# Optimization experiments

Measured on AMD Instinct MI355X. Metric: run time of the kernel, lower is better.

## Reference

```python
import jax, jax.numpy as jnp
import numpy as np

N = 50000   # nodes
E = 800000  # edges (avg degree 16)
D = 128     # feature / hidden dim


def _lin(x, W, b):
    # torch nn.Linear convention: W is [out, in]
    return x @ W.T + b


def setup_inputs() -> dict:
    key = jax.random.key(0)
    ks = jax.random.split(key, 24)
    p = lambda k, s: jax.random.normal(k, s, dtype=jnp.float32) * 0.05
    inp = {
        "node_feat": jax.random.normal(ks[0], (N, D), dtype=jnp.float32),
        "edge_feat": jax.random.normal(ks[1], (E, D), dtype=jnp.float32),
        "src_idx": jax.random.randint(ks[2], (E,), 0, N),
        "dst_idx": jax.random.randint(ks[3], (E,), 0, N),
        "Wsrc": p(ks[4], (D, D)), "bsrc": p(ks[5], (D,)),
        "Wdst": p(ks[6], (D, D)), "bdst": p(ks[7], (D,)),
        "Wphi1": p(ks[8], (D, D)), "bphi1": p(ks[9], (D,)),
        "Wphi2": p(ks[10], (D, D)), "bphi2": p(ks[11], (D,)),
        "Wphi3": p(ks[12], (D, D)), "bphi3": p(ks[13], (D,)),
        "Wth1": p(ks[14], (D, D)), "bth1": p(ks[15], (D,)),
        "Wth2": p(ks[16], (D, D)), "bth2": p(ks[17], (D,)),
        "Wpd": p(ks[18], (D, D)), "bpd": p(ks[19], (D,)),
        "Wpu": p(ks[20], (D, D)), "bpu": p(ks[21], (D,)),
    }
    return inp


def reference(node_feat, edge_feat, src_idx, dst_idx,
              Wsrc, bsrc, Wdst, bdst,
              Wphi1, bphi1, Wphi2, bphi2, Wphi3, bphi3,
              Wth1, bth1, Wth2, bth2,
              Wpd, bpd, Wpu, bpu):
    h = node_feat                               # [N, D]
    h_src = h[src_idx]                          # [E, D] gather
    h_dst = h[dst_idx]                          # [E, D] gather
    # edge code: e + affine(src) + affine(dst)
    t = edge_feat + _lin(h_src, Wsrc, bsrc) + _lin(h_dst, Wdst, bdst)
    # phi MLP (activation_first=True, n_hidden=2): ReLU, L, ReLU, L, ReLU, L
    x = jax.nn.relu(t)
    x = jax.nn.relu(_lin(x, Wphi1, bphi1))
    x = jax.nn.relu(_lin(x, Wphi2, bphi2))
    e_emb = _lin(x, Wphi3, bphi3)               # [E, D]
    # u_mul_e + sum: message = h[src] * e_emb, scatter-sum into dst
    m = h_src * e_emb                           # [E, D]
    agg = jax.ops.segment_sum(m, dst_idx, num_segments=h.shape[0])  # [N, D]
    # combine: theta(phi_dst(h) + phi_upd(agg)); theta = ReLU, L, ReLU, L
    y = _lin(h, Wpd, bpd) + _lin(agg, Wpu, bpu)
    y = jax.nn.relu(y)
    y = jax.nn.relu(_lin(y, Wth1, bth1))
    return _lin(y, Wth2, bth2)                  # [N, D]
```

## Files before the change

### kernel.cpp

```cpp
#include <hip/hip_runtime.h>
#include <hip/hip_bf16.h>

#define NN 50000
#define NE 800000
#define NT_E 12500

typedef __attribute__((ext_vector_type(8))) short bf16x8;
typedef __attribute__((ext_vector_type(4))) float f32x4;
typedef __attribute__((ext_vector_type(8))) unsigned short u16x8;

__device__ __forceinline__ unsigned short f2bf(float f) {
    union { float f; unsigned u; } v; v.f = f;
    unsigned r = v.u + 0x7FFFu + ((v.u >> 16) & 1u);
    return (unsigned short)(r >> 16);
}
__device__ __forceinline__ float bf2f(unsigned short h) {
    union { unsigned u; float f; } v; v.u = ((unsigned)h) << 16;
    return v.f;
}
__device__ __forceinline__ f32x4 mfma16(bf16x8 a, bf16x8 b, f32x4 c) {
    return __builtin_amdgcn_mfma_f32_16x16x32_bf16(a, b, c, 0, 0, 0);
}

__device__ __forceinline__ void load_wfrags(const unsigned short* __restrict__ Wb,
                                            int wv, int lane, bf16x8 (&wf)[4][2]) {
#pragma unroll
    for (int kk = 0; kk < 4; ++kk)
#pragma unroll
        for (int j = 0; j < 2; ++j) {
            int row = 32 * wv + 16 * j + (lane & 15);
            int col = 32 * kk + 8 * (lane >> 4);
            wf[kk][j] = *(const bf16x8*)(Wb + row * 128 + col);
        }
}

__device__ __forceinline__ void zero_acc(f32x4 (&acc)[4][2]) {
#pragma unroll
    for (int mt = 0; mt < 4; ++mt)
#pragma unroll
        for (int j = 0; j < 2; ++j) {
            f32x4 z = {0.f, 0.f, 0.f, 0.f};
            acc[mt][j] = z;
        }
}

__device__ __forceinline__ void gemm64(const unsigned short* __restrict__ X,
                                       const bf16x8 (&wf)[4][2], f32x4 (&acc)[4][2], int lane) {
#pragma unroll
    for (int kk = 0; kk < 4; ++kk) {
        bf16x8 a[4];
#pragma unroll
        for (int mt = 0; mt < 4; ++mt) {
            int row = mt * 16 + (lane & 15);
            a[mt] = *(const bf16x8*)(X + row * 136 + kk * 32 + 8 * (lane >> 4));
        }
#pragma unroll
        for (int mt = 0; mt < 4; ++mt) {
            acc[mt][0] = mfma16(a[mt], wf[kk][0], acc[mt][0]);
            acc[mt][1] = mfma16(a[mt], wf[kk][1], acc[mt][1]);
        }
    }
}

__device__ __forceinline__ void epi_lds(unsigned short* __restrict__ Xo,
                                        const f32x4 (&acc)[4][2],
                                        float bb0, float bb1, int c0, int rbase) {
#pragma unroll
    for (int mt = 0; mt < 4; ++mt)
#pragma unroll
        for (int r = 0; r < 4; ++r) {
            int row = mt * 16 + rbase + r;
            Xo[row * 136 + c0]      = f2bf(fmaxf(acc[mt][0][r] + bb0, 0.f));
            Xo[row * 136 + c0 + 16] = f2bf(fmaxf(acc[mt][1][r] + bb1, 0.f));
        }
}

__global__ void k_wconv(const float* w0, const float* w1, const float* w2,
                        const float* w3, const float* w4, const float* w5,
                        const float* w6, const float* w7, const float* w8,
                        unsigned short* out) {
    const float* ws[9] = {w0, w1, w2, w3, w4, w5, w6, w7, w8};
    int m = blockIdx.x >> 2;
    int part = blockIdx.x & 3;
    const float* w = ws[m] + part * 4096 + threadIdx.x * 16;
    unsigned short* o = out + m * 16384 + part * 4096 + threadIdx.x * 16;
    float f[16];
#pragma unroll
    for (int i = 0; i < 4; ++i) *(f32x4*)(f + 4 * i) = ((const f32x4*)w)[i];
    unsigned short tmp[16];
#pragma unroll
    for (int i = 0; i < 16; ++i) tmp[i] = f2bf(f[i]);
    ((u16x8*)o)[0] = *(u16x8*)tmp;
    ((u16x8*)o)[1] = *(u16x8*)(tmp + 8);
}

__global__ __launch_bounds__(256, 2)
void k_nodepre(const float* __restrict__ h,
               const unsigned short* __restrict__ Wb,
               const float* __restrict__ bsrc, const float* __restrict__ bdst,
               unsigned short* __restrict__ Asrc, unsigned short* __restrict__ Adst,
               unsigned short* __restrict__ Hb) {
    __shared__ unsigned short X[64 * 136];
    int tid = threadIdx.x, lane = tid & 63, wv = tid >> 6;
    int n0 = blockIdx.x * 64;
    {
        int row = tid >> 2, q = tid & 3;
        int n = n0 + row;
        unsigned short tmp[32];
        if (n < NN) {
            const f32x4* hp = (const f32x4*)(h + (size_t)n * 128 + q * 32);
#pragma unroll
            for (int i = 0; i < 8; ++i) {
                f32x4 v = hp[i];
#pragma unroll
                for (int j = 0; j < 4; ++j) tmp[i * 4 + j] = f2bf(v[j]);
            }
        } else {
#pragma unroll
            for (int i = 0; i < 32; ++i) tmp[i] = 0;
        }
#pragma unroll
        for (int i = 0; i < 4; ++i)
            *(u16x8*)(X + row * 136 + q * 32 + i * 8) = *(u16x8*)(tmp + i * 8);
        if (n < NN) {
            u16x8* hb = (u16x8*)(Hb + (size_t)n * 128 + q * 32);
#pragma unroll
            for (int i = 0; i < 4; ++i) hb[i] = *(u16x8*)(tmp + i * 8);
        }
    }
    __syncthreads();

    bf16x8 wfS[4][2], wfD[4][2];
    load_wfrags(Wb, wv, lane, wfS);
    load_wfrags(Wb + 16384, wv, lane, wfD);
    f32x4 accS[4][2], accD[4][2];
    zero_acc(accS); zero_acc(accD);
    gemm64(X, wfS, accS, lane);
    gemm64(X, wfD, accD, lane);

    int c0 = 32 * wv + (lane & 15);
    float bs0 = bsrc[c0], bs1 = bsrc[c0 + 16];
    float bd0 = bdst[c0], bd1 = bdst[c0 + 16];
    int rbase = (lane >> 4) * 4;
#pragma unroll
    for (int mt = 0; mt < 4; ++mt)
#pragma unroll
        for (int r = 0; r < 4; ++r) {
            int n = n0 + mt * 16 + rbase + r;
            if (n < NN) {
                size_t o = (size_t)n * 128;
                Asrc[o + c0]      = f2bf(accS[mt][0][r] + bs0);
                Asrc[o + c0 + 16] = f2bf(accS[mt][1][r] + bs1);
                Adst[o + c0]      = f2bf(accD[mt][0][r] + bd0);
                Adst[o + c0 + 16] = f2bf(accD[mt][1][r] + bd1);
            }
        }
}

__global__ __launch_bounds__(256, 2)
void k_edge(const float* __restrict__ ef,
            const int* __restrict__ src, const int* __restrict__ dst,
            const unsigned short* __restrict__ Asrc,
            const unsigned short* __restrict__ Adst,
            const unsigned short* __restrict__ Hb,
            const unsigned short* __restrict__ Wb,
            const float* __restrict__ b1, const float* __restrict__ b2,
            const float* __restrict__ b3,
            float* __restrict__ agg) {
    __shared__ unsigned short X0[64 * 136];
    __shared__ unsigned short X1[64 * 136];
    __shared__ unsigned short Hs[64 * 136];
    __shared__ int soff_lds[64];
    __shared__ int doff_lds[64];

    int tid = threadIdx.x, lane = tid & 63, wv = tid >> 6;

    bf16x8 wf1[4][2], wf2[4][2], wf3[4][2];
    load_wfrags(Wb + 2 * 16384, wv, lane, wf1);
    load_wfrags(Wb + 3 * 16384, wv, lane, wf2);
    load_wfrags(Wb + 4 * 16384, wv, lane, wf3);

    int c0 = 32 * wv + (lane & 15);
    float b1_0 = b1[c0], b1_1 = b1[c0 + 16];
    float b2_0 = b2[c0], b2_1 = b2[c0 + 16];
    float b3_0 = b3[c0], b3_1 = b3[c0 + 16];
    int rbase = (lane >> 4) * 4;
    int srow = tid >> 2, q = tid & 3;

    for (int t = blockIdx.x; t < NT_E; t += gridDim.x) {
        int e0 = t * 64;
        __syncthreads();
        if (tid < 64) {
            soff_lds[tid] = src[e0 + tid] * 128;
            doff_lds[tid] = dst[e0 + tid] * 128;
        }
        __syncthreads();
        {
            int so = soff_lds[srow], dofs = doff_lds[srow];
            const f32x4* ep = (const f32x4*)(ef + (size_t)(e0 + srow) * 128 + q * 32);
            const u16x8* ap = (const u16x8*)(Asrc + so + q * 32);
            const u16x8* dp = (const u16x8*)(Adst + dofs + q * 32);
            const u16x8* hp = (const u16x8*)(Hb + so + q * 32);
#pragma unroll
            for (int i = 0; i < 4; ++i) {
                u16x8 a8 = ap[i], d8 = dp[i], h8 = hp[i];
                f32x4 e_lo = ep[2 * i], e_hi = ep[2 * i + 1];
                unsigned short o[8];
#pragma unroll
                for (int j = 0; j < 8; ++j) {
                    float evv = (j < 4) ? e_lo[j] : e_hi[j - 4];
                    float v = evv + bf2f((unsigned short)a8[j]) + bf2f((unsigned short)d8[j]);
                    o[j] = f2bf(fmaxf(v, 0.f));
                }
                *(u16x8*)(X0 + srow * 136 + q * 32 + i * 8) = *(u16x8*)o;
                *(u16x8*)(Hs + srow * 136 + q * 32 + i * 8) = h8;
            }
        }
        __syncthreads();
        f32x4 acc[4][2];
        zero_acc(acc);
        gemm64(X0, wf1, acc, lane);
        __syncthreads();
        epi_lds(X1, acc, b1_0, b1_1, c0, rbase);
        __syncthreads();
        zero_acc(acc);
        gemm64(X1, wf2, acc, lane);
        epi_lds(X0, acc, b2_0, b2_1, c0, rbase);
        __syncthreads();
        zero_acc(acc);
        gemm64(X0, wf3, acc, lane);
#pragma unroll
        for (int mt = 0; mt < 4; ++mt)
#pragma unroll
            for (int r = 0; r < 4; ++r) {
                int row = mt * 16 + rbase + r;
                int dofs = doff_lds[row];
                float h0 = bf2f(Hs[row * 136 + c0]);
                float h1 = bf2f(Hs[row * 136 + c0 + 16]);
                atomicAdd(agg + dofs + c0,      (acc[mt][0][r] + b3_0) * h0);
                atomicAdd(agg + dofs + c0 + 16, (acc[mt][1][r] + b3_1) * h1);
            }
    }
}

__global__ __launch_bounds__(256, 2)
void k_nodeout(const unsigned short* __restrict__ Hb,
               const float* __restrict__ agg,
               const unsigned short* __restrict__ Wb,
               const float* __restrict__ bpd, const float* __restrict__ bpu,
               const float* __restrict__ bt1, const float* __restrict__ bt2,
               float* __restrict__ out) {
    __shared__ unsigned short Xh[64 * 136];
    __shared__ unsigned short Xa[64 * 136];
    int tid = threadIdx.x, lane = tid & 63, wv = tid >> 6;
    int n0 = blockIdx.x * 64;
    {
        int row = tid >> 2, q = tid & 3;
        int n = n0 + row;
        if (n < NN) {
            const u16x8* hp = (const u16x8*)(Hb + (size_t)n * 128 + q * 32);
#pragma unroll
            for (int i = 0; i < 4; ++i)
                *(u16x8*)(Xh + row * 136 + q * 32 + i * 8) = hp[i];
            const f32x4* gp = (const f32x4*)(agg + (size_t)n * 128 + q * 32);
#pragma unroll
            for (int i = 0; i < 4; ++i) {
                f32x4 lo = gp[2 * i], hi = gp[2 * i + 1];
                unsigned short tmp[8];
#pragma unroll
                for (int j = 0; j < 4; ++j) { tmp[j] = f2bf(lo[j]); tmp[4 + j] = f2bf(hi[j]); }
                *(u16x8*)(Xa + row * 136 + q * 32 + i * 8) = *(u16x8*)tmp;
            }
        } else {
            u16x8 z = {0, 0, 0, 0, 0, 0, 0, 0};
#pragma unroll
            for (int i = 0; i < 4; ++i) {
                *(u16x8*)(Xh + row * 136 + q * 32 + i * 8) = z;
                *(u16x8*)(Xa + row * 136 + q * 32 + i * 8) = z;
            }
        }
    }
    __syncthreads();
    bf16x8 wfa[4][2], wfb[4][2];
    load_wfrags(Wb + 5 * 16384, wv, lane, wfa);
    load_wfrags(Wb + 6 * 16384, wv, lane, wfb);
    int c0 = 32 * wv + (lane & 15);
    int rbase = (lane >> 4) * 4;
    f32x4 acc[4][2];
    zero_acc(acc);
    gemm64(Xh, wfa, acc, lane);
    gemm64(Xa, wfb, acc, lane);
    float bb0 = bpd[c0] + bpu[c0], bb1 = bpd[c0 + 16] + bpu[c0 + 16];
    __syncthreads();
    epi_lds(Xh, acc, bb0, bb1, c0, rbase);
    __syncthreads();
    load_wfrags(Wb + 7 * 16384, wv, lane, wfa);
    zero_acc(acc);
    gemm64(Xh, wfa, acc, lane);
    float b10 = bt1[c0], b11 = bt1[c0 + 16];
    __syncthreads();
    epi_lds(Xa, acc, b10, b11, c0, rbase);
    __syncthreads();
    load_wfrags(Wb + 8 * 16384, wv, lane, wfb);
    zero_acc(acc);
    gemm64(Xa, wfb, acc, lane);
    float b20 = bt2[c0], b21 = bt2[c0 + 16];
#pragma unroll
    for (int mt = 0; mt < 4; ++mt)
#pragma unroll
        for (int r = 0; r < 4; ++r) {
            int n = n0 + mt * 16 + rbase + r;
            if (n < NN) {
                out[(size_t)n * 128 + c0]      = acc[mt][0][r] + b20;
                out[(size_t)n * 128 + c0 + 16] = acc[mt][1][r] + b21;
            }
        }
}

extern "C" void kernel_launch(void* const* d_in, const int* in_sizes, int n_in,
                              void* d_out, int out_size, void* d_ws, size_t ws_size,
                              hipStream_t stream) {
    (void)in_sizes; (void)n_in; (void)out_size; (void)ws_size;
    const float* node_feat = (const float*)d_in[0];
    const float* edge_feat = (const float*)d_in[1];
    const int*   src  = (const int*)d_in[2];
    const int*   dst  = (const int*)d_in[3];
    const float* Wsrc = (const float*)d_in[4];  const float* bsrc = (const float*)d_in[5];
    const float* Wdst = (const float*)d_in[6];  const float* bdst = (const float*)d_in[7];
    const float* Wphi1 = (const float*)d_in[8]; const float* bphi1 = (const float*)d_in[9];
    const float* Wphi2 = (const float*)d_in[10];const float* bphi2 = (const float*)d_in[11];
    const float* Wphi3 = (const float*)d_in[12];const float* bphi3 = (const float*)d_in[13];
    const float* Wth1 = (const float*)d_in[14]; const float* bth1 = (const float*)d_in[15];
    const float* Wth2 = (const float*)d_in[16]; const float* bth2 = (const float*)d_in[17];
    const float* Wpd  = (const float*)d_in[18]; const float* bpd  = (const float*)d_in[19];
    const float* Wpu  = (const float*)d_in[20]; const float* bpu  = (const float*)d_in[21];

    char* ws = (char*)d_ws;
    unsigned short* Wb   = (unsigned short*)ws;
    unsigned short* Asrc = (unsigned short*)(ws + 294912);
    unsigned short* Adst = (unsigned short*)(ws + 294912 + 12800000);
    unsigned short* Hb   = (unsigned short*)(ws + 294912 + 25600000);
    float*          agg  = (float*)(ws + 294912 + 38400000);

    hipMemsetAsync(agg, 0, (size_t)NN * 128 * 4, stream);

    k_wconv<<<36, 256, 0, stream>>>(Wsrc, Wdst, Wphi1, Wphi2, Wphi3,
                                    Wpd, Wpu, Wth1, Wth2, Wb);
    k_nodepre<<<782, 256, 0, stream>>>(node_feat, Wb, bsrc, bdst, Asrc, Adst, Hb);
    k_edge<<<1024, 256, 0, stream>>>(edge_feat, src, dst, Asrc, Adst, Hb, Wb,
                                     bphi1, bphi2, bphi3, agg);
    k_nodeout<<<782, 256, 0, stream>>>(Hb, agg, Wb, bpd, bpu, bth1, bth2, (float*)d_out);
}
```

Baseline: 468.3 us.

## Sort edges by destination and pre-reduce messages in LDS before atomics

Builds a destination-sorted edge permutation each call using a histogram, a single-block scan and an atomic-cursor scatter. The edge kernel then processes edges in that order with contiguous tile ranges per block, and reduces runs of equal destinations through shared memory so far fewer global atomics hit agg. It also drops the bf16 copy of node features: the edge kernel gathers fp32 node_feat directly and converts it, and occupancy rises to 3 blocks. Costs are three extra small kernels, indirect, uncoalesced reads of edge_feat through the permutation, and wider fp32 gathers for h_src.

```diff
diff --git a/kernel.cpp b/kernel.cpp
--- a/kernel.cpp
+++ b/kernel.cpp
@@ -73,6 +73,18 @@
             Xo[row * 136 + c0]      = f2bf(fmaxf(acc[mt][0][r] + bb0, 0.f));
             Xo[row * 136 + c0 + 16] = f2bf(fmaxf(acc[mt][1][r] + bb1, 0.f));
         }
+}
+
+__device__ __forceinline__ void stage_f32row(unsigned short* __restrict__ Xrow,
+                                             const f32x4* __restrict__ p) {
+#pragma unroll
+    for (int i = 0; i < 4; ++i) {
+        f32x4 lo = p[2 * i], hi = p[2 * i + 1];
+        unsigned short tmp[8];
+#pragma unroll
+        for (int j = 0; j < 4; ++j) { tmp[j] = f2bf(lo[j]); tmp[4 + j] = f2bf(hi[j]); }
+        *(u16x8*)(Xrow + i * 8) = *(u16x8*)tmp;
+    }
 }
 
 __global__ void k_wconv(const float* w0, const float* w1, const float* w2,
@@ -94,38 +106,62 @@
     ((u16x8*)o)[1] = *(u16x8*)(tmp + 8);
 }
 
-__global__ __launch_bounds__(256, 2)
+__global__ void k_hist(const int* __restrict__ dst, int* __restrict__ cnt) {
+    int i = blockIdx.x * 256 + threadIdx.x;
+    int stride = gridDim.x * 256;
+    for (; i < NE; i += stride) atomicAdd(&cnt[dst[i]], 1);
+}
+
+__global__ void k_scan(int* __restrict__ c) {
+    __shared__ int part[1024];
+    int tid = threadIdx.x;
+    const int CH = 49;
+    int base = tid * CH;
+    int s = 0;
+    for (int i = 0; i < CH; ++i) { int idx = base + i; if (idx < NN) s += c[idx]; }
+    part[tid] = s;
+    __syncthreads();
+    for (int off = 1; off < 1024; off <<= 1) {
+        int v = (tid >= off) ? part[tid - off] : 0;
+        __syncthreads();
+        part[tid] += v;
+        __syncthreads();
+    }
+    int excl = (tid == 0) ? 0 : part[tid - 1];
+    for (int i = 0; i < CH; ++i) {
+        int idx = base + i;
+        if (idx < NN) { int cc = c[idx]; c[idx] = excl; excl += cc; }
+    }
+}
+
+__global__ void k_perm(const int* __restrict__ dst, int* __restrict__ cursor,
+                       int* __restrict__ perm) {
+    int i = blockIdx.x * 256 + threadIdx.x;
+    int stride = gridDim.x * 256;
+    for (; i < NE; i += stride) {
+        int p = atomicAdd(&cursor[dst[i]], 1);
+        perm[p] = i;
+    }
+}
+
+__global__ __launch_bounds__(256, 3)
 void k_nodepre(const float* __restrict__ h,
                const unsigned short* __restrict__ Wb,
                const float* __restrict__ bsrc, const float* __restrict__ bdst,
-               unsigned short* __restrict__ Asrc, unsigned short* __restrict__ Adst,
-               unsigned short* __restrict__ Hb) {
+               unsigned short* __restrict__ Asrc, unsigned short* __restrict__ Adst) {
     __shared__ unsigned short X[64 * 136];
     int tid = threadIdx.x, lane = tid & 63, wv = tid >> 6;
     int n0 = blockIdx.x * 64;
     {
         int row = tid >> 2, q = tid & 3;
         int n = n0 + row;
-        unsigned short tmp[32];
         if (n < NN) {
-            const f32x4* hp = (const f32x4*)(h + (size_t)n * 128 + q * 32);
-#pragma unroll
-            for (int i = 0; i < 8; ++i) {
-                f32x4 v = hp[i];
-#pragma unroll
-                for (int j = 0; j < 4; ++j) tmp[i * 4 + j] = f2bf(v[j]);
-            }
+            stage_f32row(X + row * 136 + q * 32,
+                         (const f32x4*)(h + (size_t)n * 128 + q * 32));
         } else {
-#pragma unroll
-            for (int i = 0; i < 32; ++i) tmp[i] = 0;
-        }
-#pragma unroll
-        for (int i = 0; i < 4; ++i)
-            *(u16x8*)(X + row * 136 + q * 32 + i * 8) = *(u16x8*)(tmp + i * 8);
-        if (n < NN) {
-            u16x8* hb = (u16x8*)(Hb + (size_t)n * 128 + q * 32);
-#pragma unroll
-            for (int i = 0; i < 4; ++i) hb[i] = *(u16x8*)(tmp + i * 8);
+            u16x8 z = {0, 0, 0, 0, 0, 0, 0, 0};
+#pragma unroll
+            for (int i = 0; i < 4; ++i) *(u16x8*)(X + row * 136 + q * 32 + i * 8) = z;
         }
     }
     __syncthreads();
@@ -157,21 +193,25 @@
         }
 }
 
-__global__ __launch_bounds__(256, 2)
+__global__ __launch_bounds__(256, 3)
 void k_edge(const float* __restrict__ ef,
+            const float* __restrict__ nf,
             const int* __restrict__ src, const int* __restrict__ dst,
+            const int* __restrict__ perm,
             const unsigned short* __restrict__ Asrc,
             const unsigned short* __restrict__ Adst,
-            const unsigned short* __restrict__ Hb,
             const unsigned short* __restrict__ Wb,
             const float* __restrict__ b1, const float* __restrict__ b2,
             const float* __restrict__ b3,
             float* __restrict__ agg) {
-    __shared__ unsigned short X0[64 * 136];
-    __shared__ unsigned short X1[64 * 136];
-    __shared__ unsigned short Hs[64 * 136];
-    __shared__ int soff_lds[64];
-    __shared__ int doff_lds[64];
+    __shared__ __align__(16) char sh[52992];
+    unsigned short* X0 = (unsigned short*)sh;
+    unsigned short* X1 = (unsigned short*)(sh + 17408);
+    float*          Mf = (float*)sh;
+    unsigned short* Hs = (unsigned short*)(sh + 34816);
+    int* soff = (int*)(sh + 52224);
+    int* didx = (int*)(sh + 52480);
+    int* eidx = (int*)(sh + 52736);
 
     int tid = threadIdx.x, lane = tid & 63, wv = tid >> 6;
 
@@ -187,33 +227,45 @@
     int rbase = (lane >> 4) * 4;
     int srow = tid >> 2, q = tid & 3;
 
-    for (int t = blockIdx.x; t < NT_E; t += gridDim.x) {
+    int b = blockIdx.x, nb = gridDim.x;
+    int qt = NT_E / nb, rt = NT_E % nb;
+    int t0 = (b < rt) ? b * (qt + 1) : rt * (qt + 1) + (b - rt) * qt;
+    int t1 = t0 + ((b < rt) ? qt + 1 : qt);
+
+    for (int t = t0; t < t1; ++t) {
         int e0 = t * 64;
         __syncthreads();
         if (tid < 64) {
-            soff_lds[tid] = src[e0 + tid] * 128;
-            doff_lds[tid] = dst[e0 + tid] * 128;
+            int e = perm[e0 + tid];
+            eidx[tid] = e;
+            soff[tid] = src[e] * 128;
+            didx[tid] = dst[e];
         }
         __syncthreads();
         {
-            int so = soff_lds[srow], dofs = doff_lds[srow];
-            const f32x4* ep = (const f32x4*)(ef + (size_t)(e0 + srow) * 128 + q * 32);
+            int e = eidx[srow];
+            int so = soff[srow];
+            int dofs = didx[srow] * 128;
+            const f32x4* ep = (const f32x4*)(ef + (size_t)e * 128 + q * 32);
+            const f32x4* hp = (const f32x4*)(nf + (size_t)so + q * 32);
             const u16x8* ap = (const u16x8*)(Asrc + so + q * 32);
             const u16x8* dp = (const u16x8*)(Adst + dofs + q * 32);
-            const u16x8* hp = (const u16x8*)(Hb + so + q * 32);
 #pragma unroll
             for (int i = 0; i < 4; ++i) {
-                u16x8 a8 = ap[i], d8 = dp[i], h8 = hp[i];
+                u16x8 a8 = ap[i], d8 = dp[i];
                 f32x4 e_lo = ep[2 * i], e_hi = ep[2 * i + 1];
-                unsigned short o[8];
+                f32x4 h_lo = hp[2 * i], h_hi = hp[2 * i + 1];
+                unsigned short o[8], hb[8];
 #pragma unroll
                 for (int j = 0; j < 8; ++j) {
                     float evv = (j < 4) ? e_lo[j] : e_hi[j - 4];
+                    float hv  = (j < 4) ? h_lo[j] : h_hi[j - 4];
                     float v = evv + bf2f((unsigned short)a8[j]) + bf2f((unsigned short)d8[j]);
                     o[j] = f2bf(fmaxf(v, 0.f));
+                    hb[j] = f2bf(hv);
                 }
                 *(u16x8*)(X0 + srow * 136 + q * 32 + i * 8) = *(u16x8*)o;
-                *(u16x8*)(Hs + srow * 136 + q * 32 + i * 8) = h8;
+                *(u16x8*)(Hs + srow * 136 + q * 32 + i * 8) = *(u16x8*)hb;
             }
         }
         __syncthreads();
@@ -229,22 +281,38 @@
         __syncthreads();
         zero_acc(acc);
         gemm64(X0, wf3, acc, lane);
+        __syncthreads();
 #pragma unroll
         for (int mt = 0; mt < 4; ++mt)
 #pragma unroll
             for (int r = 0; r < 4; ++r) {
                 int row = mt * 16 + rbase + r;
-                int dofs = doff_lds[row];
                 float h0 = bf2f(Hs[row * 136 + c0]);
                 float h1 = bf2f(Hs[row * 136 + c0 + 16]);
-                atomicAdd(agg + dofs + c0,      (acc[mt][0][r] + b3_0) * h0);
-                atomicAdd(agg + dofs + c0 + 16, (acc[mt][1][r] + b3_1) * h1);
-            }
-    }
-}
-
-__global__ __launch_bounds__(256, 2)
-void k_nodeout(const unsigned short* __restrict__ Hb,
+                Mf[row * 128 + c0]      = (acc[mt][0][r] + b3_0) * h0;
+                Mf[row * 128 + c0 + 16] = (acc[mt][1][r] + b3_1) * h1;
+            }
+        __syncthreads();
+        {
+            int col = tid & 127;
+            int r0 = (tid >> 7) * 32;
+            float s = 0.f;
+            int cur = didx[r0];
+            for (int r = r0; r < r0 + 32; ++r) {
+                int d2 = didx[r];
+                if (d2 != cur) {
+                    atomicAdd(agg + (size_t)cur * 128 + col, s);
+                    s = 0.f; cur = d2;
+                }
+                s += Mf[r * 128 + col];
+            }
+            atomicAdd(agg + (size_t)cur * 128 + col, s);
+        }
+    }
+}
+
+__global__ __launch_bounds__(256, 3)
+void k_nodeout(const float* __restrict__ h,
                const float* __restrict__ agg,
                const unsigned short* __restrict__ Wb,
                const float* __restrict__ bpd, const float* __restrict__ bpu,
@@ -258,19 +326,10 @@
         int row = tid >> 2, q = tid & 3;
         int n = n0 + row;
         if (n < NN) {
-            const u16x8* hp = (const u16x8*)(Hb + (size_t)n * 128 + q * 32);
-#pragma unroll
-            for (int i = 0; i < 4; ++i)
-                *(u16x8*)(Xh + row * 136 + q * 32 + i * 8) = hp[i];
-            const f32x4* gp = (const f32x4*)(agg + (size_t)n * 128 + q * 32);
-#pragma unroll
-            for (int i = 0; i < 4; ++i) {
-                f32x4 lo = gp[2 * i], hi = gp[2 * i + 1];
-                unsigned short tmp[8];
-#pragma unroll
-                for (int j = 0; j < 4; ++j) { tmp[j] = f2bf(lo[j]); tmp[4 + j] = f2bf(hi[j]); }
-                *(u16x8*)(Xa + row * 136 + q * 32 + i * 8) = *(u16x8*)tmp;
-            }
+            stage_f32row(Xh + row * 136 + q * 32,
+                         (const f32x4*)(h + (size_t)n * 128 + q * 32));
+            stage_f32row(Xa + row * 136 + q * 32,
+                         (const f32x4*)(agg + (size_t)n * 128 + q * 32));
         } else {
             u16x8 z = {0, 0, 0, 0, 0, 0, 0, 0};
 #pragma unroll
@@ -338,16 +397,22 @@
     char* ws = (char*)d_ws;
     unsigned short* Wb   = (unsigned short*)ws;
     unsigned short* Asrc = (unsigned short*)(ws + 294912);
-    unsigned short* Adst = (unsigned short*)(ws + 294912 + 12800000);
-    unsigned short* Hb   = (unsigned short*)(ws + 294912 + 25600000);
-    float*          agg  = (float*)(ws + 294912 + 38400000);
+    unsigned short* Adst = (unsigned short*)(ws + 13094912);
+    float*          agg  = (float*)(ws + 25894912);
+    int*            perm = (int*)(ws + 51494912);
+    int*            cnt  = (int*)(ws + 54694912);
 
     hipMemsetAsync(agg, 0, (size_t)NN * 128 * 4, stream);
+    hipMemsetAsync(cnt, 0, (size_t)NN * 4, stream);
 
     k_wconv<<<36, 256, 0, stream>>>(Wsrc, Wdst, Wphi1, Wphi2, Wphi3,
                                     Wpd, Wpu, Wth1, Wth2, Wb);
-    k_nodepre<<<782, 256, 0, stream>>>(node_feat, Wb, bsrc, bdst, Asrc, Adst, Hb);
-    k_edge<<<1024, 256, 0, stream>>>(edge_feat, src, dst, Asrc, Adst, Hb, Wb,
-                                     bphi1, bphi2, bphi3, agg);
-    k_nodeout<<<782, 256, 0, stream>>>(Hb, agg, Wb, bpd, bpu, bth1, bth2, (float*)d_out);
-}
+    k_hist<<<1024, 256, 0, stream>>>(dst, cnt);
+    k_scan<<<1, 1024, 0, stream>>>(cnt);
+    k_perm<<<1024, 256, 0, stream>>>(dst, cnt, perm);
+    k_nodepre<<<782, 256, 0, stream>>>(node_feat, Wb, bsrc, bdst, Asrc, Adst);
+    k_edge<<<1024, 256, 0, stream>>>(edge_feat, node_feat, src, dst, perm,
+                                     Asrc, Adst, Wb, bphi1, bphi2, bphi3, agg);
+    k_nodeout<<<782, 256, 0, stream>>>(node_feat, agg, Wb, bpd, bpu, bth1, bth2,
+                                       (float*)d_out);
+}
```

Result: slower. 923.9 us (+97.3%).

## Replace atomic scatter with CSR-sorted message buffer and segmented reduction

Applied to the files above, without the earlier changes.

Builds a CSR of destinations each call (histogram, three-stage scan, position assignment). The edge kernel writes bf16 messages into a dst-sorted buffer instead of issuing float atomics, and a separate per-node kernel then sums each segment without atomics. The edge kernel also prefetches the next tile's gathers into registers to overlap them with the MLP, and occupancy hints rise to 3 blocks. This costs extra launches, a large extra buffer of writes and reads, and bf16 rounding of messages. It falls back to the atomic path when the workspace is too small.

```diff
diff --git a/kernel.cpp b/kernel.cpp
--- a/kernel.cpp
+++ b/kernel.cpp
@@ -4,10 +4,14 @@
 #define NN 50000
 #define NE 800000
 #define NT_E 12500
+#define GRID_E 1536
+#define NBLK_SCAN 196
 
 typedef __attribute__((ext_vector_type(8))) short bf16x8;
 typedef __attribute__((ext_vector_type(4))) float f32x4;
+typedef __attribute__((ext_vector_type(2))) float f32x2;
 typedef __attribute__((ext_vector_type(8))) unsigned short u16x8;
+typedef __attribute__((ext_vector_type(2))) unsigned short u16x2;
 
 __device__ __forceinline__ unsigned short f2bf(float f) {
     union { float f; unsigned u; } v; v.f = f;
@@ -21,6 +25,9 @@
 __device__ __forceinline__ f32x4 mfma16(bf16x8 a, bf16x8 b, f32x4 c) {
     return __builtin_amdgcn_mfma_f32_16x16x32_bf16(a, b, c, 0, 0, 0);
 }
+__device__ __forceinline__ void syncl() {
+    asm volatile("s_waitcnt lgkmcnt(0)\n\ts_barrier" ::: "memory");
+}
 
 __device__ __forceinline__ void load_wfrags(const unsigned short* __restrict__ Wb,
                                             int wv, int lane, bf16x8 (&wf)[4][2]) {
@@ -73,6 +80,18 @@
             Xo[row * 136 + c0]      = f2bf(fmaxf(acc[mt][0][r] + bb0, 0.f));
             Xo[row * 136 + c0 + 16] = f2bf(fmaxf(acc[mt][1][r] + bb1, 0.f));
         }
+}
+
+__device__ __forceinline__ void stage_f32row(unsigned short* __restrict__ Xrow,
+                                             const f32x4* __restrict__ p) {
+#pragma unroll
+    for (int i = 0; i < 4; ++i) {
+        f32x4 lo = p[2 * i], hi = p[2 * i + 1];
+        unsigned short tmp[8];
+#pragma unroll
+        for (int j = 0; j < 4; ++j) { tmp[j] = f2bf(lo[j]); tmp[4 + j] = f2bf(hi[j]); }
+        *(u16x8*)(Xrow + i * 8) = *(u16x8*)tmp;
+    }
 }
 
 __global__ void k_wconv(const float* w0, const float* w1, const float* w2,
@@ -94,7 +113,63 @@
     ((u16x8*)o)[1] = *(u16x8*)(tmp + 8);
 }
 
-__global__ __launch_bounds__(256, 2)
+__global__ void k_hist(const int* __restrict__ dst, int* __restrict__ cnt) {
+    int i = blockIdx.x * 256 + threadIdx.x;
+    if (i < NE) atomicAdd(&cnt[dst[i]], 1);
+}
+
+__global__ void k_scan1(const int* __restrict__ c, int* __restrict__ bsum) {
+    __shared__ int red[256];
+    int i = blockIdx.x * 256 + threadIdx.x;
+    red[threadIdx.x] = (i < NN) ? c[i] : 0;
+    __syncthreads();
+    for (int off = 128; off > 0; off >>= 1) {
+        if (threadIdx.x < off) red[threadIdx.x] += red[threadIdx.x + off];
+        __syncthreads();
+    }
+    if (threadIdx.x == 0) bsum[blockIdx.x] = red[0];
+}
+
+__global__ void k_scan2(int* __restrict__ bsum) {
+    __shared__ int s[256];
+    int t = threadIdx.x;
+    s[t] = (t < NBLK_SCAN) ? bsum[t] : 0;
+    __syncthreads();
+    for (int off = 1; off < 256; off <<= 1) {
+        int v = (t >= off) ? s[t - off] : 0;
+        __syncthreads();
+        s[t] += v;
+        __syncthreads();
+    }
+    if (t < NBLK_SCAN) bsum[t] = (t == 0) ? 0 : s[t - 1];
+}
+
+__global__ void k_scan3(int* __restrict__ cnt, const int* __restrict__ bsum,
+                        int* __restrict__ rowptr) {
+    __shared__ int s[256];
+    int t = threadIdx.x;
+    int i = blockIdx.x * 256 + t;
+    int v = (i < NN) ? cnt[i] : 0;
+    s[t] = v;
+    __syncthreads();
+    for (int off = 1; off < 256; off <<= 1) {
+        int x = (t >= off) ? s[t - off] : 0;
+        __syncthreads();
+        s[t] += x;
+        __syncthreads();
+    }
+    int excl = bsum[blockIdx.x] + s[t] - v;
+    if (i < NN) { rowptr[i] = excl; cnt[i] = excl; }
+    if (i == 0) rowptr[NN] = NE;
+}
+
+__global__ void k_pos(const int* __restrict__ dst, int* __restrict__ cursor,
+                      int* __restrict__ pos) {
+    int i = blockIdx.x * 256 + threadIdx.x;
+    if (i < NE) pos[i] = atomicAdd(&cursor[dst[i]], 1);
+}
+
+__global__ __launch_bounds__(256, 3)
 void k_nodepre(const float* __restrict__ h,
                const unsigned short* __restrict__ Wb,
                const float* __restrict__ bsrc, const float* __restrict__ bdst,
@@ -106,8 +181,8 @@
     {
         int row = tid >> 2, q = tid & 3;
         int n = n0 + row;
-        unsigned short tmp[32];
         if (n < NN) {
+            unsigned short tmp[32];
             const f32x4* hp = (const f32x4*)(h + (size_t)n * 128 + q * 32);
 #pragma unroll
             for (int i = 0; i < 8; ++i) {
@@ -115,17 +190,16 @@
 #pragma unroll
                 for (int j = 0; j < 4; ++j) tmp[i * 4 + j] = f2bf(v[j]);
             }
+#pragma unroll
+            for (int i = 0; i < 4; ++i)
+                *(u16x8*)(X + row * 136 + q * 32 + i * 8) = *(u16x8*)(tmp + i * 8);
+            u16x8* hb = (u16x8*)(Hb + (size_t)n * 128 + q * 32);
+#pragma unroll
+            for (int i = 0; i < 4; ++i) hb[i] = *(u16x8*)(tmp + i * 8);
         } else {
-#pragma unroll
-            for (int i = 0; i < 32; ++i) tmp[i] = 0;
-        }
-#pragma unroll
-        for (int i = 0; i < 4; ++i)
-            *(u16x8*)(X + row * 136 + q * 32 + i * 8) = *(u16x8*)(tmp + i * 8);
-        if (n < NN) {
-            u16x8* hb = (u16x8*)(Hb + (size_t)n * 128 + q * 32);
-#pragma unroll
-            for (int i = 0; i < 4; ++i) hb[i] = *(u16x8*)(tmp + i * 8);
+            u16x8 z = {0, 0, 0, 0, 0, 0, 0, 0};
+#pragma unroll
+            for (int i = 0; i < 4; ++i) *(u16x8*)(X + row * 136 + q * 32 + i * 8) = z;
         }
     }
     __syncthreads();
@@ -157,16 +231,156 @@
         }
 }
 
+__global__ __launch_bounds__(256, 3)
+void k_edgeA(const float* __restrict__ ef,
+             const int* __restrict__ src, const int* __restrict__ dst,
+             const int* __restrict__ pos,
+             const unsigned short* __restrict__ Asrc,
+             const unsigned short* __restrict__ Adst,
+             const unsigned short* __restrict__ Hb,
+             const unsigned short* __restrict__ Wb,
+             const float* __restrict__ b1, const float* __restrict__ b2,
+             const float* __restrict__ b3,
+             unsigned short* __restrict__ Mbuf) {
+    __shared__ __align__(16) char sh[52480];
+    unsigned short* X0 = (unsigned short*)sh;
+    unsigned short* X1 = (unsigned short*)(sh + 17408);
+    unsigned short* Hs = (unsigned short*)(sh + 34816);
+    float*          Mf = (float*)sh;
+    int*         posarr = (int*)(sh + 52224);
+
+    int tid = threadIdx.x, lane = tid & 63, wv = tid >> 6;
+
+    bf16x8 wf1[4][2], wf2[4][2], wf3[4][2];
+    load_wfrags(Wb + 2 * 16384, wv, lane, wf1);
+    load_wfrags(Wb + 3 * 16384, wv, lane, wf2);
+    load_wfrags(Wb + 4 * 16384, wv, lane, wf3);
+
+    int c0 = 32 * wv + (lane & 15);
+    float b1_0 = b1[c0], b1_1 = b1[c0 + 16];
+    float b2_0 = b2[c0], b2_1 = b2[c0 + 16];
+    float b3_0 = b3[c0], b3_1 = b3[c0 + 16];
+    int rbase = (lane >> 4) * 4;
+    int srow = tid >> 2, q = tid & 3;
+
+    int e_nx, s_nx, d_nx, p_nx;
+    f32x4 efr[8];
+    u16x8 asr[4], adr[4], hbr[4];
+
+    auto load_idx = [&](int t) {
+        int e = t * 64 + srow;
+        e_nx = e;
+        s_nx = src[e]; d_nx = dst[e]; p_nx = pos[e];
+    };
+    auto load_gather = [&]() {
+        const f32x4* ep = (const f32x4*)(ef + (size_t)e_nx * 128 + q * 32);
+#pragma unroll
+        for (int i = 0; i < 8; ++i) efr[i] = ep[i];
+        const u16x8* ap = (const u16x8*)(Asrc + (size_t)s_nx * 128 + q * 32);
+        const u16x8* dp = (const u16x8*)(Adst + (size_t)d_nx * 128 + q * 32);
+        const u16x8* hp = (const u16x8*)(Hb + (size_t)s_nx * 128 + q * 32);
+#pragma unroll
+        for (int i = 0; i < 4; ++i) { asr[i] = ap[i]; adr[i] = dp[i]; hbr[i] = hp[i]; }
+    };
+
+    int t0 = blockIdx.x;
+    load_idx(t0);
+    load_gather();
+
+    for (int t = t0; t < NT_E; t += GRID_E) {
+        int tn = t + GRID_E;
+        syncl();
+        {
+#pragma unroll
+            for (int i = 0; i < 4; ++i) {
+                u16x8 a8 = asr[i], d8 = adr[i];
+                f32x4 lo = efr[2 * i], hi = efr[2 * i + 1];
+                unsigned short o[8];
+#pragma unroll
+                for (int j = 0; j < 8; ++j) {
+                    float evv = (j < 4) ? lo[j] : hi[j - 4];
+                    float v = evv + bf2f((unsigned short)a8[j]) + bf2f((unsigned short)d8[j]);
+                    o[j] = f2bf(fmaxf(v, 0.f));
+                }
+                *(u16x8*)(X0 + srow * 136 + q * 32 + i * 8) = *(u16x8*)o;
+                *(u16x8*)(Hs + srow * 136 + q * 32 + i * 8) = hbr[i];
+            }
+            if (q == 0) posarr[srow] = p_nx;
+        }
+        if (tn < NT_E) load_idx(tn);
+        syncl();
+        if (tn < NT_E) load_gather();
+
+        f32x4 acc[4][2];
+        zero_acc(acc);
+        gemm64(X0, wf1, acc, lane);
+        syncl();
+        epi_lds(X1, acc, b1_0, b1_1, c0, rbase);
+        syncl();
+        zero_acc(acc);
+        gemm64(X1, wf2, acc, lane);
+        epi_lds(X0, acc, b2_0, b2_1, c0, rbase);
+        syncl();
+        zero_acc(acc);
+        gemm64(X0, wf3, acc, lane);
+        syncl();
+#pragma unroll
+        for (int mt = 0; mt < 4; ++mt)
+#pragma unroll
+            for (int r = 0; r < 4; ++r) {
+                int row = mt * 16 + rbase + r;
+                float h0 = bf2f(Hs[row * 136 + c0]);
+                float h1 = bf2f(Hs[row * 136 + c0 + 16]);
+                Mf[row * 128 + c0]      = (acc[mt][0][r] + b3_0) * h0;
+                Mf[row * 128 + c0 + 16] = (acc[mt][1][r] + b3_1) * h1;
+            }
+        syncl();
+#pragma unroll
+        for (int i = 0; i < 16; ++i) {
+            int row = wv * 16 + i;
+            int posr = posarr[row];
+            f32x2 v = *(const f32x2*)(Mf + row * 128 + lane * 2);
+            u16x2 o2; o2[0] = f2bf(v[0]); o2[1] = f2bf(v[1]);
+            *(u16x2*)(Mbuf + (size_t)posr * 128 + lane * 2) = o2;
+        }
+    }
+}
+
+__global__ __launch_bounds__(256)
+void k_agg(const unsigned short* __restrict__ Mbuf,
+           const int* __restrict__ rowptr, float* __restrict__ agg) {
+    int n = (blockIdx.x * 256 + threadIdx.x) >> 6;
+    int lane = threadIdx.x & 63;
+    if (n >= NN) return;
+    int j0 = rowptr[n], j1 = rowptr[n + 1];
+    float a0 = 0.f, a1 = 0.f;
+    int j = j0;
+    for (; j + 3 < j1; j += 4) {
+        u16x2 v0 = *(const u16x2*)(Mbuf + (size_t)j * 128 + lane * 2);
+        u16x2 v1 = *(const u16x2*)(Mbuf + (size_t)(j + 1) * 128 + lane * 2);
+        u16x2 v2 = *(const u16x2*)(Mbuf + (size_t)(j + 2) * 128 + lane * 2);
+        u16x2 v3 = *(const u16x2*)(Mbuf + (size_t)(j + 3) * 128 + lane * 2);
+        a0 += bf2f(v0[0]) + bf2f(v1[0]) + bf2f(v2[0]) + bf2f(v3[0]);
+        a1 += bf2f(v0[1]) + bf2f(v1[1]) + bf2f(v2[1]) + bf2f(v3[1]);
+    }
+    for (; j < j1; ++j) {
+        u16x2 v = *(const u16x2*)(Mbuf + (size_t)j * 128 + lane * 2);
+        a0 += bf2f(v[0]); a1 += bf2f(v[1]);
+    }
+    f32x2 o; o[0] = a0; o[1] = a1;
+    *(f32x2*)(agg + (size_t)n * 128 + lane * 2) = o;
+}
+
 __global__ __launch_bounds__(256, 2)
-void k_edge(const float* __restrict__ ef,
-            const int* __restrict__ src, const int* __restrict__ dst,
-            const unsigned short* __restrict__ Asrc,
-            const unsigned short* __restrict__ Adst,
-            const unsigned short* __restrict__ Hb,
-            const unsigned short* __restrict__ Wb,
-            const float* __restrict__ b1, const float* __restrict__ b2,
-            const float* __restrict__ b3,
-            float* __restrict__ agg) {
+void k_edge_atomic(const float* __restrict__ ef,
+                   const int* __restrict__ src, const int* __restrict__ dst,
+                   const unsigned short* __restrict__ Asrc,
+                   const unsigned short* __restrict__ Adst,
+                   const unsigned short* __restrict__ Hb,
+                   const unsigned short* __restrict__ Wb,
+                   const float* __restrict__ b1, const float* __restrict__ b2,
+                   const float* __restrict__ b3,
+                   float* __restrict__ agg) {
     __shared__ unsigned short X0[64 * 136];
     __shared__ unsigned short X1[64 * 136];
     __shared__ unsigned short Hs[64 * 136];
@@ -174,7 +388,6 @@
     __shared__ int doff_lds[64];
 
     int tid = threadIdx.x, lane = tid & 63, wv = tid >> 6;
-
     bf16x8 wf1[4][2], wf2[4][2], wf3[4][2];
     load_wfrags(Wb + 2 * 16384, wv, lane, wf1);
     load_wfrags(Wb + 3 * 16384, wv, lane, wf2);
@@ -243,7 +456,7 @@
     }
 }
 
-__global__ __launch_bounds__(256, 2)
+__global__ __launch_bounds__(256, 3)
 void k_nodeout(const unsigned short* __restrict__ Hb,
                const float* __restrict__ agg,
                const unsigned short* __restrict__ Wb,
@@ -262,15 +475,8 @@
 #pragma unroll
             for (int i = 0; i < 4; ++i)
                 *(u16x8*)(Xh + row * 136 + q * 32 + i * 8) = hp[i];
-            const f32x4* gp = (const f32x4*)(agg + (size_t)n * 128 + q * 32);
-#pragma unroll
-            for (int i = 0; i < 4; ++i) {
-                f32x4 lo = gp[2 * i], hi = gp[2 * i + 1];
-                unsigned short tmp[8];
-#pragma unroll
-                for (int j = 0; j < 4; ++j) { tmp[j] = f2bf(lo[j]); tmp[4 + j] = f2bf(hi[j]); }
-                *(u16x8*)(Xa + row * 136 + q * 32 + i * 8) = *(u16x8*)tmp;
-            }
+            stage_f32row(Xa + row * 136 + q * 32,
+                         (const f32x4*)(agg + (size_t)n * 128 + q * 32));
         } else {
             u16x8 z = {0, 0, 0, 0, 0, 0, 0, 0};
 #pragma unroll
@@ -320,7 +526,7 @@
 extern "C" void kernel_launch(void* const* d_in, const int* in_sizes, int n_in,
                               void* d_out, int out_size, void* d_ws, size_t ws_size,
                               hipStream_t stream) {
-    (void)in_sizes; (void)n_in; (void)out_size; (void)ws_size;
+    (void)in_sizes; (void)n_in; (void)out_size;
     const float* node_feat = (const float*)d_in[0];
     const float* edge_feat = (const float*)d_in[1];
     const int*   src  = (const int*)d_in[2];
@@ -336,18 +542,40 @@
     const float* Wpu  = (const float*)d_in[20]; const float* bpu  = (const float*)d_in[21];
 
     char* ws = (char*)d_ws;
-    unsigned short* Wb   = (unsigned short*)ws;
-    unsigned short* Asrc = (unsigned short*)(ws + 294912);
-    unsigned short* Adst = (unsigned short*)(ws + 294912 + 12800000);
-    unsigned short* Hb   = (unsigned short*)(ws + 294912 + 25600000);
-    float*          agg  = (float*)(ws + 294912 + 38400000);
-
-    hipMemsetAsync(agg, 0, (size_t)NN * 128 * 4, stream);
+    size_t off = 0;
+    unsigned short* Wb   = (unsigned short*)(ws + off); off += 294912;
+    unsigned short* Asrc = (unsigned short*)(ws + off); off += 12800000;
+    unsigned short* Adst = (unsigned short*)(ws + off); off += 12800000;
+    unsigned short* Hb   = (unsigned short*)(ws + off); off += 12800000;
+    float*          agg  = (float*)(ws + off);          off += 25600000;
+    int*            cnt  = (int*)(ws + off);            off += 200064;
+    int*            rowptr = (int*)(ws + off);          off += 200064;
+    int*            bsum = (int*)(ws + off);            off += 1024;
+    int*            pos  = (int*)(ws + off);            off += 3200000;
+    unsigned short* Mbuf = (unsigned short*)(ws + off); off += 204800000;
+    bool primary = (ws_size >= off);
 
     k_wconv<<<36, 256, 0, stream>>>(Wsrc, Wdst, Wphi1, Wphi2, Wphi3,
                                     Wpd, Wpu, Wth1, Wth2, Wb);
     k_nodepre<<<782, 256, 0, stream>>>(node_feat, Wb, bsrc, bdst, Asrc, Adst, Hb);
-    k_edge<<<1024, 256, 0, stream>>>(edge_feat, src, dst, Asrc, Adst, Hb, Wb,
-                                     bphi1, bphi2, bphi3, agg);
-    k_nodeout<<<782, 256, 0, stream>>>(Hb, agg, Wb, bpd, bpu, bth1, bth2, (float*)d_out);
-}
+
+    if (primary) {
+        hipMemsetAsync(cnt, 0, (size_t)NN * 4, stream);
+        k_hist<<<3125, 256, 0, stream>>>(dst, cnt);
+        k_scan1<<<NBLK_SCAN, 256, 0, stream>>>(cnt, bsum);
+        k_scan2<<<1, 256, 0, stream>>>(bsum);
+        k_scan3<<<NBLK_SCAN, 256, 0, stream>>>(cnt, bsum, rowptr);
+        k_pos<<<3125, 256, 0, stream>>>(dst, cnt, pos);
+        k_edgeA<<<GRID_E, 256, 0, stream>>>(edge_feat, src, dst, pos,
+                                            Asrc, Adst, Hb, Wb,
+                                            bphi1, bphi2, bphi3, Mbuf);
+        k_agg<<<(NN * 64 + 255) / 256, 256, 0, stream>>>(Mbuf, rowptr, agg);
+    } else {
+        hipMemsetAsync(agg, 0, (size_t)NN * 128 * 4, stream);
+        k_edge_atomic<<<1024, 256, 0, stream>>>(edge_feat, src, dst,
+                                                Asrc, Adst, Hb, Wb,
+                                                bphi1, bphi2, bphi3, agg);
+    }
+    k_nodeout<<<782, 256, 0, stream>>>(Hb, agg, Wb, bpd, bpu, bth1, bth2,
+                                       (float*)d_out);
+}
```

After: 787.5 us. 1.68x slower.
